# Kernel tuning notes

Measured on AMD Instinct MI355X. Metric: run time of the kernel, lower is better.

The kernel has to match this reference:

```python
import jax, jax.numpy as jnp
import numpy as np

H = 100

def _lstm_cell(x_t, h, c, Wi, Wh, bi, bh):
    # gates: [B, 4H]; PyTorch LSTMCell gate order = i, f, g, o
    g = x_t @ Wi.T + bi + h @ Wh.T + bh
    i, f, gg, o = jnp.split(g, 4, axis=-1)
    c_new = jax.nn.sigmoid(f) * c + jax.nn.sigmoid(i) * jnp.tanh(gg)
    h_new = jax.nn.sigmoid(o) * jnp.tanh(c_new)
    return h_new, c_new


def setup_inputs() -> dict:
    key = jax.random.key(0)
    ks = jax.random.split(key, 11)
    B, T = 2048, 256
    s1 = 1.0 / np.sqrt(H)
    d = {
        "x": jax.random.normal(ks[0], (B, T), dtype=jnp.float32),
        "W_ih1": jax.random.uniform(ks[1], (4 * H, 1), jnp.float32, -s1, s1),
        "W_hh1": jax.random.uniform(ks[2], (4 * H, H), jnp.float32, -s1, s1),
        "b_ih1": jax.random.uniform(ks[3], (4 * H,), jnp.float32, -s1, s1),
        "b_hh1": jax.random.uniform(ks[4], (4 * H,), jnp.float32, -s1, s1),
        "W_ih2": jax.random.uniform(ks[5], (4 * H, H), jnp.float32, -s1, s1),
        "W_hh2": jax.random.uniform(ks[6], (4 * H, H), jnp.float32, -s1, s1),
        "b_ih2": jax.random.uniform(ks[7], (4 * H,), jnp.float32, -s1, s1),
        "b_hh2": jax.random.uniform(ks[8], (4 * H,), jnp.float32, -s1, s1),
        "W_lin": jax.random.uniform(ks[9], (1, H), jnp.float32, -s1, s1),
        "b_lin": jax.random.uniform(ks[10], (1,), jnp.float32, -s1, s1),
    }
    return d


def reference(x, W_ih1, W_hh1, b_ih1, b_hh1, W_ih2, W_hh2, b_ih2, b_hh2, W_lin, b_lin):
    B = x.shape[0]
    zeros = jnp.zeros((B, H), dtype=x.dtype)
    init = (zeros, zeros, zeros, zeros)  # h1, c1, h2, c2
    xs = x.T[:, :, None]  # [T, B, 1]

    def step(carry, x_t):
        h1, c1, h2, c2 = carry
        h1, c1 = _lstm_cell(x_t, h1, c1, W_ih1, W_hh1, b_ih1, b_hh1)
        h2, c2 = _lstm_cell(h1, h2, c2, W_ih2, W_hh2, b_ih2, b_hh2)
        return (h1, c1, h2, c2), None

    (h1, c1, h2, c2), _ = jax.lax.scan(step, init, xs)
    return h2 @ W_lin.T + b_lin  # [B, 1]
```

## Files before the change

kernel.cpp:

```cpp
#include <hip/hip_runtime.h>

#define T_STEPS 256
#define HH      100
#define ROWS    8
#define NMV     500
#define BLK     512

#define WS_TOTAL 121301

__global__ __launch_bounds__(512) void pack_kernel(
    const float* __restrict__ Whh1, const float* __restrict__ Wih2,
    const float* __restrict__ Whh2,
    const float* __restrict__ bih1, const float* __restrict__ bhh1,
    const float* __restrict__ bih2, const float* __restrict__ bhh2,
    const float* __restrict__ Wih1, const float* __restrict__ Wlin,
    const float* __restrict__ blin, float* __restrict__ ws) {
  int idx = blockIdx.x * BLK + threadIdx.x;
  if (idx < 120000) {
    int kk = idx & 3;
    int q  = idx >> 2;
    int t  = q % 500;
    int q2 = q / 500;
    int i  = q2 % 5;
    int q3 = q2 / 5;
    int c  = q3 & 3;
    int m  = q3 >> 2;
    int s  = t / 100;
    int j  = t - s * 100;
    int col = c * 100 + j;
    int k   = s * 20 + i * 4 + kk;
    const float* W = (m == 0) ? Whh1 : (m == 1) ? Wih2 : Whh2;
    ws[idx] = W[col * HH + k];
  } else if (idx < 120400) {
    int j = idx - 120000; ws[idx] = bih1[j] + bhh1[j];
  } else if (idx < 120800) {
    int j = idx - 120400; ws[idx] = bih2[j] + bhh2[j];
  } else if (idx < 121200) {
    ws[idx] = Wih1[idx - 120800];
  } else if (idx < 121300) {
    ws[idx] = Wlin[idx - 121200];
  } else if (idx == 121300) {
    ws[idx] = blin[0];
  }
}

__device__ __forceinline__ float sigf(float v) {
  return 1.0f / (1.0f + __expf(-v));
}
__device__ __forceinline__ float tanh_fast(float v) {
  float t = __expf(2.0f * v);
  return 1.0f - 2.0f / (t + 1.0f);
}

__device__ __forceinline__ void mv4(const float* __restrict__ wp, int mbase,
                                    const float (*__restrict__ hb)[HH],
                                    int s20, float acc[4][8]) {
#pragma unroll
  for (int i = 0; i < 5; ++i) {
    float4 w0 = *(const float4*)(wp + (mbase +  0 + i) * 2000);
    float4 w1 = *(const float4*)(wp + (mbase +  5 + i) * 2000);
    float4 w2 = *(const float4*)(wp + (mbase + 10 + i) * 2000);
    float4 w3 = *(const float4*)(wp + (mbase + 15 + i) * 2000);
#pragma unroll
    for (int r = 0; r < 8; ++r) {
      float4 h = *(const float4*)&hb[r][s20 + i * 4];
      acc[0][r] = fmaf(w0.x, h.x, fmaf(w0.y, h.y, fmaf(w0.z, h.z, fmaf(w0.w, h.w, acc[0][r]))));
      acc[1][r] = fmaf(w1.x, h.x, fmaf(w1.y, h.y, fmaf(w1.z, h.z, fmaf(w1.w, h.w, acc[1][r]))));
      acc[2][r] = fmaf(w2.x, h.x, fmaf(w2.y, h.y, fmaf(w2.z, h.z, fmaf(w2.w, h.w, acc[2][r]))));
      acc[3][r] = fmaf(w3.x, h.x, fmaf(w3.y, h.y, fmaf(w3.z, h.z, fmaf(w3.w, h.w, acc[3][r]))));
    }
  }
}

__global__ __launch_bounds__(512) void lstm_persist(
    const float* __restrict__ x, const float* __restrict__ ws,
    float* __restrict__ out, int T) {
  __shared__ float gbp[5][ROWS][400];
  __shared__ __align__(16) float h1[ROWS][HH];
  __shared__ __align__(16) float h2[ROWS][HH];
  __shared__ float b1s[400], b2s[400], wis[400], wls[HH], xs[ROWS];

  const int tid = threadIdx.x;
  const int r0  = blockIdx.x * ROWS;

  if (tid < 400) {
    b1s[tid] = ws[120000 + tid];
    b2s[tid] = ws[120400 + tid];
    wis[tid] = ws[120800 + tid];
  }
  if (tid < HH) wls[tid] = ws[121200 + tid];
#pragma unroll
  for (int p = 0; p < 2; ++p) {
    int e = tid + 512 * p;
    if (e < ROWS * HH) { (&h1[0][0])[e] = 0.0f; (&h2[0][0])[e] = 0.0f; }
  }
  if (tid < ROWS) xs[tid] = x[(r0 + tid) * T];
  __syncthreads();

  const bool mv  = (tid < NMV);
  const int  s   = tid / 100;
  const int  j   = tid - s * 100;
  const int  s20 = s * 20;
  const float* wp = ws + tid * 4;

  const int e0r = tid / 100, e0n = tid - e0r * 100;
  const int e1  = tid + 512;
  const int e1r = e1 / 100, e1n = e1 - e1r * 100;
  const bool a1 = (e1 < ROWS * HH);
  float c1a = 0.f, c1b = 0.f, c2a = 0.f, c2b = 0.f;

#pragma unroll 1
  for (int t = 0; t < T; ++t) {
    if (mv) {
      float acc[4][8];
#pragma unroll
      for (int c = 0; c < 4; ++c)
#pragma unroll
        for (int r = 0; r < 8; ++r) acc[c][r] = 0.0f;
      mv4(wp, 0, h1, s20, acc);
#pragma unroll
      for (int c = 0; c < 4; ++c)
#pragma unroll
        for (int r = 0; r < 8; ++r) gbp[s][r][c * 100 + j] = acc[c][r];
    }
    __syncthreads();

    {
      {
        float xv = xs[e0r];
        float g[4];
#pragma unroll
        for (int gg = 0; gg < 4; ++gg) {
          int jj = e0n + 100 * gg;
          float v = gbp[0][e0r][jj] + gbp[1][e0r][jj] + gbp[2][e0r][jj] +
                    gbp[3][e0r][jj] + gbp[4][e0r][jj];
          g[gg] = v + b1s[jj] + wis[jj] * xv;
        }
        float iv = sigf(g[0]), fv = sigf(g[1]);
        float gv = tanh_fast(g[2]), ov = sigf(g[3]);
        c1a = fv * c1a + iv * gv;
        h1[e0r][e0n] = ov * tanh_fast(c1a);
      }
      if (a1) {
        float xv = xs[e1r];
        float g[4];
#pragma unroll
        for (int gg = 0; gg < 4; ++gg) {
          int jj = e1n + 100 * gg;
          float v = gbp[0][e1r][jj] + gbp[1][e1r][jj] + gbp[2][e1r][jj] +
                    gbp[3][e1r][jj] + gbp[4][e1r][jj];
          g[gg] = v + b1s[jj] + wis[jj] * xv;
        }
        float iv = sigf(g[0]), fv = sigf(g[1]);
        float gv = tanh_fast(g[2]), ov = sigf(g[3]);
        c1b = fv * c1b + iv * gv;
        h1[e1r][e1n] = ov * tanh_fast(c1b);
      }
    }
    __syncthreads();

    if (mv) {
      float acc[4][8];
#pragma unroll
      for (int c = 0; c < 4; ++c)
#pragma unroll
        for (int r = 0; r < 8; ++r) acc[c][r] = 0.0f;
      mv4(wp, 20, h1, s20, acc);
      mv4(wp, 40, h2, s20, acc);
#pragma unroll
      for (int c = 0; c < 4; ++c)
#pragma unroll
        for (int r = 0; r < 8; ++r) gbp[s][r][c * 100 + j] = acc[c][r];
    }
    __syncthreads();

    {
      {
        float g[4];
#pragma unroll
        for (int gg = 0; gg < 4; ++gg) {
          int jj = e0n + 100 * gg;
          float v = gbp[0][e0r][jj] + gbp[1][e0r][jj] + gbp[2][e0r][jj] +
                    gbp[3][e0r][jj] + gbp[4][e0r][jj];
          g[gg] = v + b2s[jj];
        }
        float iv = sigf(g[0]), fv = sigf(g[1]);
        float gv = tanh_fast(g[2]), ov = sigf(g[3]);
        c2a = fv * c2a + iv * gv;
        h2[e0r][e0n] = ov * tanh_fast(c2a);
      }
      if (a1) {
        float g[4];
#pragma unroll
        for (int gg = 0; gg < 4; ++gg) {
          int jj = e1n + 100 * gg;
          float v = gbp[0][e1r][jj] + gbp[1][e1r][jj] + gbp[2][e1r][jj] +
                    gbp[3][e1r][jj] + gbp[4][e1r][jj];
          g[gg] = v + b2s[jj];
        }
        float iv = sigf(g[0]), fv = sigf(g[1]);
        float gv = tanh_fast(g[2]), ov = sigf(g[3]);
        c2b = fv * c2b + iv * gv;
        h2[e1r][e1n] = ov * tanh_fast(c2b);
      }
    }
    if (tid < ROWS && (t + 1) < T) xs[tid] = x[(r0 + tid) * T + t + 1];
    __syncthreads();
  }

  {
    int row  = tid >> 6;
    int lane = tid & 63;
    float p = h2[row][lane] * wls[lane];
    if (lane + 64 < HH) p += h2[row][lane + 64] * wls[lane + 64];
#pragma unroll
    for (int off = 32; off > 0; off >>= 1) p += __shfl_down(p, off, 64);
    if (lane == 0) out[r0 + row] = p + ws[121300];
  }
}

extern "C" void kernel_launch(void* const* d_in, const int* in_sizes, int n_in,
                              void* d_out, int out_size, void* d_ws, size_t ws_size,
                              hipStream_t stream) {
  const float* x    = (const float*)d_in[0];
  const float* Wih1 = (const float*)d_in[1];
  const float* Whh1 = (const float*)d_in[2];
  const float* bih1 = (const float*)d_in[3];
  const float* bhh1 = (const float*)d_in[4];
  const float* Wih2 = (const float*)d_in[5];
  const float* Whh2 = (const float*)d_in[6];
  const float* bih2 = (const float*)d_in[7];
  const float* bhh2 = (const float*)d_in[8];
  const float* Wlin = (const float*)d_in[9];
  const float* blin = (const float*)d_in[10];

  float* ws  = (float*)d_ws;
  float* out = (float*)d_out;

  const int B = in_sizes[0] / T_STEPS;

  pack_kernel<<<(WS_TOTAL + BLK - 1) / BLK, BLK, 0, stream>>>(
      Whh1, Wih2, Whh2, bih1, bhh1, bih2, bhh2, Wih1, Wlin, blin, ws);

  lstm_persist<<<B / ROWS, BLK, 0, stream>>>(x, ws, out, T_STEPS);
}
```

Baseline: 2.696 ms.

## Keep layer-1 recurrent weights in registers and prefetch layer-2 weights

```diff
diff --git a/kernel.cpp b/kernel.cpp
--- a/kernel.cpp
+++ b/kernel.cpp
@@ -51,25 +51,8 @@
   float t = __expf(2.0f * v);
   return 1.0f - 2.0f / (t + 1.0f);
 }
-
-__device__ __forceinline__ void mv4(const float* __restrict__ wp, int mbase,
-                                    const float (*__restrict__ hb)[HH],
-                                    int s20, float acc[4][8]) {
-#pragma unroll
-  for (int i = 0; i < 5; ++i) {
-    float4 w0 = *(const float4*)(wp + (mbase +  0 + i) * 2000);
-    float4 w1 = *(const float4*)(wp + (mbase +  5 + i) * 2000);
-    float4 w2 = *(const float4*)(wp + (mbase + 10 + i) * 2000);
-    float4 w3 = *(const float4*)(wp + (mbase + 15 + i) * 2000);
-#pragma unroll
-    for (int r = 0; r < 8; ++r) {
-      float4 h = *(const float4*)&hb[r][s20 + i * 4];
-      acc[0][r] = fmaf(w0.x, h.x, fmaf(w0.y, h.y, fmaf(w0.z, h.z, fmaf(w0.w, h.w, acc[0][r]))));
-      acc[1][r] = fmaf(w1.x, h.x, fmaf(w1.y, h.y, fmaf(w1.z, h.z, fmaf(w1.w, h.w, acc[1][r]))));
-      acc[2][r] = fmaf(w2.x, h.x, fmaf(w2.y, h.y, fmaf(w2.z, h.z, fmaf(w2.w, h.w, acc[2][r]))));
-      acc[3][r] = fmaf(w3.x, h.x, fmaf(w3.y, h.y, fmaf(w3.z, h.z, fmaf(w3.w, h.w, acc[3][r]))));
-    }
-  }
+__device__ __forceinline__ void fma4(const float4 w, const float4 h, float& a) {
+  a = fmaf(w.x, h.x, fmaf(w.y, h.y, fmaf(w.z, h.z, fmaf(w.w, h.w, a))));
 }
 
 __global__ __launch_bounds__(512) void lstm_persist(
@@ -103,21 +86,47 @@
   const int  s20 = s * 20;
   const float* wp = ws + tid * 4;
 
+  float4 p1w[4][5];
+  if (mv) {
+#pragma unroll
+    for (int g = 0; g < 4; ++g)
+#pragma unroll
+      for (int i = 0; i < 5; ++i)
+        p1w[g][i] = *(const float4*)(wp + (g * 5 + i) * 2000);
+  }
+
   const int e0r = tid / 100, e0n = tid - e0r * 100;
   const int e1  = tid + 512;
   const int e1r = e1 / 100, e1n = e1 - e1r * 100;
   const bool a1 = (e1 < ROWS * HH);
   float c1a = 0.f, c1b = 0.f, c2a = 0.f, c2b = 0.f;
 
+  float4 buf[4][4];
+
 #pragma unroll 1
   for (int t = 0; t < T; ++t) {
     if (mv) {
+#pragma unroll
+      for (int c = 0; c < 4; ++c)
+#pragma unroll
+        for (int g = 0; g < 4; ++g)
+          buf[c][g] = *(const float4*)(wp + (20 + g * 5 + c) * 2000);
+
       float acc[4][8];
 #pragma unroll
       for (int c = 0; c < 4; ++c)
 #pragma unroll
         for (int r = 0; r < 8; ++r) acc[c][r] = 0.0f;
-      mv4(wp, 0, h1, s20, acc);
+#pragma unroll
+      for (int i = 0; i < 5; ++i)
+#pragma unroll
+        for (int r = 0; r < 8; ++r) {
+          float4 h = *(const float4*)&h1[r][s20 + i * 4];
+          fma4(p1w[0][i], h, acc[0][r]);
+          fma4(p1w[1][i], h, acc[1][r]);
+          fma4(p1w[2][i], h, acc[2][r]);
+          fma4(p1w[3][i], h, acc[3][r]);
+        }
 #pragma unroll
       for (int c = 0; c < 4; ++c)
 #pragma unroll
@@ -165,8 +174,29 @@
       for (int c = 0; c < 4; ++c)
 #pragma unroll
         for (int r = 0; r < 8; ++r) acc[c][r] = 0.0f;
-      mv4(wp, 20, h1, s20, acc);
-      mv4(wp, 40, h2, s20, acc);
+
+#pragma unroll
+      for (int c = 0; c < 10; ++c) {
+        const int slot = c & 3;
+        const int ii   = (c < 5) ? c : c - 5;
+#pragma unroll
+        for (int r = 0; r < 8; ++r) {
+          float4 h = (c < 5) ? *(const float4*)&h1[r][s20 + ii * 4]
+                             : *(const float4*)&h2[r][s20 + ii * 4];
+          fma4(buf[slot][0], h, acc[0][r]);
+          fma4(buf[slot][1], h, acc[1][r]);
+          fma4(buf[slot][2], h, acc[2][r]);
+          fma4(buf[slot][3], h, acc[3][r]);
+        }
+        if (c + 4 < 10) {
+          const int c2 = c + 4;
+          const int mb = (c2 < 5) ? 20 : 40;
+          const int i2 = (c2 < 5) ? c2 : c2 - 5;
+#pragma unroll
+          for (int g = 0; g < 4; ++g)
+            buf[c2 & 3][g] = *(const float4*)(wp + (mb + g * 5 + i2) * 2000);
+        }
+      }
 #pragma unroll
       for (int c = 0; c < 4; ++c)
 #pragma unroll
```

Result: slower. 4.935 ms (+83.1%).

## Stream LSTM weights through LDS with async global_load_lds triple buffering

Applied to the files above, without the earlier changes.

```diff
diff --git a/kernel.cpp b/kernel.cpp
--- a/kernel.cpp
+++ b/kernel.cpp
@@ -1,4 +1,5 @@
 #include <hip/hip_runtime.h>
+#include <stdint.h>
 
 #define T_STEPS 256
 #define HH      100
@@ -51,34 +52,41 @@
   float t = __expf(2.0f * v);
   return 1.0f - 2.0f / (t + 1.0f);
 }
-
-__device__ __forceinline__ void mv4(const float* __restrict__ wp, int mbase,
-                                    const float (*__restrict__ hb)[HH],
-                                    int s20, float acc[4][8]) {
-#pragma unroll
-  for (int i = 0; i < 5; ++i) {
-    float4 w0 = *(const float4*)(wp + (mbase +  0 + i) * 2000);
-    float4 w1 = *(const float4*)(wp + (mbase +  5 + i) * 2000);
-    float4 w2 = *(const float4*)(wp + (mbase + 10 + i) * 2000);
-    float4 w3 = *(const float4*)(wp + (mbase + 15 + i) * 2000);
-#pragma unroll
-    for (int r = 0; r < 8; ++r) {
-      float4 h = *(const float4*)&hb[r][s20 + i * 4];
-      acc[0][r] = fmaf(w0.x, h.x, fmaf(w0.y, h.y, fmaf(w0.z, h.z, fmaf(w0.w, h.w, acc[0][r]))));
-      acc[1][r] = fmaf(w1.x, h.x, fmaf(w1.y, h.y, fmaf(w1.z, h.z, fmaf(w1.w, h.w, acc[1][r]))));
-      acc[2][r] = fmaf(w2.x, h.x, fmaf(w2.y, h.y, fmaf(w2.z, h.z, fmaf(w2.w, h.w, acc[2][r]))));
-      acc[3][r] = fmaf(w3.x, h.x, fmaf(w3.y, h.y, fmaf(w3.z, h.z, fmaf(w3.w, h.w, acc[3][r]))));
-    }
-  }
-}
+__device__ __forceinline__ void fma4(const float4 w, const float4 h, float& a) {
+  a = fmaf(w.x, h.x, fmaf(w.y, h.y, fmaf(w.z, h.z, fmaf(w.w, h.w, a))));
+}
+
+typedef const __attribute__((address_space(1))) uint32_t gu32;
+typedef __attribute__((address_space(3))) uint32_t lu32;
+__device__ __forceinline__ void stage16(const float* g, float* s) {
+  __builtin_amdgcn_global_load_lds((gu32*)g, (lu32*)s, 16, 0, 0);
+}
+
+#define L_STG 0
+#define L_GBP 12288
+#define L_H1  28288
+#define L_H2  29088
+#define L_B1  29888
+#define L_B2  30288
+#define L_WI  30688
+#define L_WL  31088
+#define L_XS  31188
+#define L_TOT 31200
+
 
 __global__ __launch_bounds__(512) void lstm_persist(
     const float* __restrict__ x, const float* __restrict__ ws,
     float* __restrict__ out, int T) {
-  __shared__ float gbp[5][ROWS][400];
-  __shared__ __align__(16) float h1[ROWS][HH];
-  __shared__ __align__(16) float h2[ROWS][HH];
-  __shared__ float b1s[400], b2s[400], wis[400], wls[HH], xs[ROWS];
+  extern __shared__ float sm[];
+  float* stg = sm + L_STG;
+  float* gbp = sm + L_GBP;
+  float* h1  = sm + L_H1;
+  float* h2  = sm + L_H2;
+  float* b1s = sm + L_B1;
+  float* b2s = sm + L_B2;
+  float* wis = sm + L_WI;
+  float* wls = sm + L_WL;
+  float* xs  = sm + L_XS;
 
   const int tid = threadIdx.x;
   const int r0  = blockIdx.x * ROWS;
@@ -89,19 +97,24 @@
     wis[tid] = ws[120800 + tid];
   }
   if (tid < HH) wls[tid] = ws[121200 + tid];
-#pragma unroll
-  for (int p = 0; p < 2; ++p) {
-    int e = tid + 512 * p;
-    if (e < ROWS * HH) { (&h1[0][0])[e] = 0.0f; (&h2[0][0])[e] = 0.0f; }
-  }
+  for (int e = tid; e < ROWS * HH; e += BLK) { h1[e] = 0.0f; h2[e] = 0.0f; }
   if (tid < ROWS) xs[tid] = x[(r0 + tid) * T];
+
+  const bool mvt = (tid < NMV);
+  const int  s   = tid / 100;
+  const int  s20 = s * 20;
+  const int  j   = tid - s * 100;
+  const float* wp = ws + tid * 4;
+  const int tid4 = tid * 4;
+  const int wb4  = (tid & 448) * 4;
+
+  if (mvt) {
+    stage16(wp +  0 * 2000, stg + (0 * 2 + 0) * 2048 + wb4);
+    stage16(wp +  5 * 2000, stg + (0 * 2 + 1) * 2048 + wb4);
+    stage16(wp + 10 * 2000, stg + (1 * 2 + 0) * 2048 + wb4);
+    stage16(wp + 15 * 2000, stg + (1 * 2 + 1) * 2048 + wb4);
+  }
   __syncthreads();
-
-  const bool mv  = (tid < NMV);
-  const int  s   = tid / 100;
-  const int  j   = tid - s * 100;
-  const int  s20 = s * 20;
-  const float* wp = ws + tid * 4;
 
   const int e0r = tid / 100, e0n = tid - e0r * 100;
   const int e1  = tid + 512;
@@ -111,17 +124,47 @@
 
 #pragma unroll 1
   for (int t = 0; t < T; ++t) {
-    if (mv) {
+    {
       float acc[4][8];
 #pragma unroll
       for (int c = 0; c < 4; ++c)
 #pragma unroll
         for (int r = 0; r < 8; ++r) acc[c][r] = 0.0f;
-      mv4(wp, 0, h1, s20, acc);
-#pragma unroll
-      for (int c = 0; c < 4; ++c)
-#pragma unroll
-        for (int r = 0; r < 8; ++r) gbp[s][r][c * 100 + j] = acc[c][r];
+#pragma unroll
+      for (int n = 0; n < 10; ++n) {
+        {
+          const int n2 = n + 2;
+          const int m2 = n2 / 10, i2 = (n2 % 10) >> 1, gp2 = (n2 & 1) * 2;
+          const int sl2 = n2 % 3;
+          if (mvt) {
+            stage16(wp + (m2 * 20 + (gp2 + 0) * 5 + i2) * 2000,
+                    stg + (sl2 * 2 + 0) * 2048 + wb4);
+            stage16(wp + (m2 * 20 + (gp2 + 1) * 5 + i2) * 2000,
+                    stg + (sl2 * 2 + 1) * 2048 + wb4);
+          }
+        }
+        asm volatile("s_waitcnt vmcnt(4)" ::: "memory");
+        __builtin_amdgcn_sched_barrier(0);
+        if (mvt) {
+          const int i = n >> 1, gp = (n & 1) * 2, sl = n % 3;
+          const float4 wa = *(const float4*)&stg[(sl * 2 + 0) * 2048 + tid4];
+          const float4 wb = *(const float4*)&stg[(sl * 2 + 1) * 2048 + tid4];
+          const int ho = s20 + i * 4;
+#pragma unroll
+          for (int r = 0; r < 8; ++r) {
+            const float4 h = *(const float4*)&h1[r * HH + ho];
+            fma4(wa, h, acc[gp][r]);
+            fma4(wb, h, acc[gp + 1][r]);
+          }
+        }
+      }
+      if (mvt) {
+#pragma unroll
+        for (int c = 0; c < 4; ++c)
+#pragma unroll
+          for (int r = 0; r < 8; ++r)
+            gbp[(s * 8 + r) * 400 + c * 100 + j] = acc[c][r];
+      }
     }
     __syncthreads();
 
@@ -132,14 +175,15 @@
 #pragma unroll
         for (int gg = 0; gg < 4; ++gg) {
           int jj = e0n + 100 * gg;
-          float v = gbp[0][e0r][jj] + gbp[1][e0r][jj] + gbp[2][e0r][jj] +
-                    gbp[3][e0r][jj] + gbp[4][e0r][jj];
+          float v = gbp[(0 * 8 + e0r) * 400 + jj] + gbp[(1 * 8 + e0r) * 400 + jj] +
+                    gbp[(2 * 8 + e0r) * 400 + jj] + gbp[(3 * 8 + e0r) * 400 + jj] +
+                    gbp[(4 * 8 + e0r) * 400 + jj];
           g[gg] = v + b1s[jj] + wis[jj] * xv;
         }
         float iv = sigf(g[0]), fv = sigf(g[1]);
         float gv = tanh_fast(g[2]), ov = sigf(g[3]);
         c1a = fv * c1a + iv * gv;
-        h1[e0r][e0n] = ov * tanh_fast(c1a);
+        h1[e0r * HH + e0n] = ov * tanh_fast(c1a);
       }
       if (a1) {
         float xv = xs[e1r];
@@ -147,30 +191,61 @@
 #pragma unroll
         for (int gg = 0; gg < 4; ++gg) {
           int jj = e1n + 100 * gg;
-          float v = gbp[0][e1r][jj] + gbp[1][e1r][jj] + gbp[2][e1r][jj] +
-                    gbp[3][e1r][jj] + gbp[4][e1r][jj];
+          float v = gbp[(0 * 8 + e1r) * 400 + jj] + gbp[(1 * 8 + e1r) * 400 + jj] +
+                    gbp[(2 * 8 + e1r) * 400 + jj] + gbp[(3 * 8 + e1r) * 400 + jj] +
+                    gbp[(4 * 8 + e1r) * 400 + jj];
           g[gg] = v + b1s[jj] + wis[jj] * xv;
         }
         float iv = sigf(g[0]), fv = sigf(g[1]);
         float gv = tanh_fast(g[2]), ov = sigf(g[3]);
         c1b = fv * c1b + iv * gv;
-        h1[e1r][e1n] = ov * tanh_fast(c1b);
+        h1[e1r * HH + e1n] = ov * tanh_fast(c1b);
       }
     }
     __syncthreads();
 
-    if (mv) {
+    {
       float acc[4][8];
 #pragma unroll
       for (int c = 0; c < 4; ++c)
 #pragma unroll
         for (int r = 0; r < 8; ++r) acc[c][r] = 0.0f;
-      mv4(wp, 20, h1, s20, acc);
-      mv4(wp, 40, h2, s20, acc);
-#pragma unroll
-      for (int c = 0; c < 4; ++c)
-#pragma unroll
-        for (int r = 0; r < 8; ++r) gbp[s][r][c * 100 + j] = acc[c][r];
+#pragma unroll
+      for (int n = 10; n < 30; ++n) {
+        {
+          const int n2 = (n + 2) % 30;
+          const int m2 = n2 / 10, i2 = (n2 % 10) >> 1, gp2 = (n2 & 1) * 2;
+          const int sl2 = n2 % 3;
+          if (mvt) {
+            stage16(wp + (m2 * 20 + (gp2 + 0) * 5 + i2) * 2000,
+                    stg + (sl2 * 2 + 0) * 2048 + wb4);
+            stage16(wp + (m2 * 20 + (gp2 + 1) * 5 + i2) * 2000,
+                    stg + (sl2 * 2 + 1) * 2048 + wb4);
+          }
+        }
+        asm volatile("s_waitcnt vmcnt(4)" ::: "memory");
+        __builtin_amdgcn_sched_barrier(0);
+        if (mvt) {
+          const int i = (n % 10) >> 1, gp = (n & 1) * 2, sl = n % 3;
+          const float4 wa = *(const float4*)&stg[(sl * 2 + 0) * 2048 + tid4];
+          const float4 wb = *(const float4*)&stg[(sl * 2 + 1) * 2048 + tid4];
+          const int ho = s20 + i * 4;
+          const float* hb = (n < 20) ? h1 : h2;
+#pragma unroll
+          for (int r = 0; r < 8; ++r) {
+            const float4 h = *(const float4*)&hb[r * HH + ho];
+            fma4(wa, h, acc[gp][r]);
+            fma4(wb, h, acc[gp + 1][r]);
+          }
+        }
+      }
+      if (mvt) {
+#pragma unroll
+        for (int c = 0; c < 4; ++c)
+#pragma unroll
+          for (int r = 0; r < 8; ++r)
+            gbp[(s * 8 + r) * 400 + c * 100 + j] = acc[c][r];
+      }
     }
     __syncthreads();
 
@@ -180,28 +255,30 @@
 #pragma unroll
         for (int gg = 0; gg < 4; ++gg) {
           int jj = e0n + 100 * gg;
-          float v = gbp[0][e0r][jj] + gbp[1][e0r][jj] + gbp[2][e0r][jj] +
-                    gbp[3][e0r][jj] + gbp[4][e0r][jj];
+          float v = gbp[(0 * 8 + e0r) * 400 + jj] + gbp[(1 * 8 + e0r) * 400 + jj] +
+                    gbp[(2 * 8 + e0r) * 400 + jj] + gbp[(3 * 8 + e0r) * 400 + jj] +
+                    gbp[(4 * 8 + e0r) * 400 + jj];
           g[gg] = v + b2s[jj];
         }
         float iv = sigf(g[0]), fv = sigf(g[1]);
         float gv = tanh_fast(g[2]), ov = sigf(g[3]);
         c2a = fv * c2a + iv * gv;
-        h2[e0r][e0n] = ov * tanh_fast(c2a);
+        h2[e0r * HH + e0n] = ov * tanh_fast(c2a);
       }
       if (a1) {
         float g[4];
 #pragma unroll
         for (int gg = 0; gg < 4; ++gg) {
           int jj = e1n + 100 * gg;
-          float v = gbp[0][e1r][jj] + gbp[1][e1r][jj] + gbp[2][e1r][jj] +
-                    gbp[3][e1r][jj] + gbp[4][e1r][jj];
+          float v = gbp[(0 * 8 + e1r) * 400 + jj] + gbp[(1 * 8 + e1r) * 400 + jj] +
+                    gbp[(2 * 8 + e1r) * 400 + jj] + gbp[(3 * 8 + e1r) * 400 + jj] +
+                    gbp[(4 * 8 + e1r) * 400 + jj];
           g[gg] = v + b2s[jj];
         }
         float iv = sigf(g[0]), fv = sigf(g[1]);
         float gv = tanh_fast(g[2]), ov = sigf(g[3]);
         c2b = fv * c2b + iv * gv;
-        h2[e1r][e1n] = ov * tanh_fast(c2b);
+        h2[e1r * HH + e1n] = ov * tanh_fast(c2b);
       }
     }
     if (tid < ROWS && (t + 1) < T) xs[tid] = x[(r0 + tid) * T + t + 1];
@@ -211,8 +288,8 @@
   {
     int row  = tid >> 6;
     int lane = tid & 63;
-    float p = h2[row][lane] * wls[lane];
-    if (lane + 64 < HH) p += h2[row][lane + 64] * wls[lane + 64];
+    float p = h2[row * HH + lane] * wls[lane];
+    if (lane + 64 < HH) p += h2[row * HH + lane + 64] * wls[lane + 64];
 #pragma unroll
     for (int off = 32; off > 0; off >>= 1) p += __shfl_down(p, off, 64);
     if (lane == 0) out[r0 + row] = p + ws[121300];
@@ -242,5 +319,5 @@
   pack_kernel<<<(WS_TOTAL + BLK - 1) / BLK, BLK, 0, stream>>>(
       Whh1, Wih2, Whh2, bih1, bhh1, bih2, bhh2, Wih1, Wlin, blin, ws);
 
-  lstm_persist<<<B / ROWS, BLK, 0, stream>>>(x, ws, out, T_STEPS);
-}
+  lstm_persist<<<B / ROWS, BLK, L_TOT * 4, stream>>>(x, ws, out, T_STEPS);
+}
```

Result: slower. 3.415 ms (+26.7%).
